# Kernel optimization log

Hardware: AMD Instinct MI355X
Metric: run time of the kernel (lower is better)

Reference implementation:

```python
import jax, jax.numpy as jnp
import numpy as np

BBOX_STD_DEV = jnp.array([0.1, 0.1, 0.2, 0.2], dtype=jnp.float32)
MIN_CONF = 0.15          # hardcoded in source (tf.where(probs >= 0.15))
NMS_THR = 0.3            # config.DETECTION_NMS_THRESHOLD
MAX_INST = 100           # config.DETECTION_MAX_INSTANCES
B, N = 8, 2048


def apply_box_deltas(boxes, deltas):
    # boxes: [N,4] (y1,x1,y2,x2); deltas: [N,4] (dy,dx,log dh,log dw)
    h = boxes[:, 2] - boxes[:, 0]
    w = boxes[:, 3] - boxes[:, 1]
    cy = boxes[:, 0] + 0.5 * h + deltas[:, 0] * h
    cx = boxes[:, 1] + 0.5 * w + deltas[:, 1] * w
    h = h * jnp.exp(deltas[:, 2])
    w = w * jnp.exp(deltas[:, 3])
    y1 = cy - 0.5 * h
    x1 = cx - 0.5 * w
    return jnp.stack([y1, x1, y1 + h, x1 + w], axis=1)


def clip_boxes(boxes, window):
    wy1, wx1, wy2, wx2 = window[0], window[1], window[2], window[3]
    y1 = jnp.clip(boxes[:, 0], wy1, wy2)
    x1 = jnp.clip(boxes[:, 1], wx1, wx2)
    y2 = jnp.clip(boxes[:, 2], wy1, wy2)
    x2 = jnp.clip(boxes[:, 3], wx1, wx2)
    return jnp.stack([y1, x1, y2, x2], axis=1)


def pairwise_iou(boxes):
    # boxes: [N,4] -> iou: [N,N]
    y1, x1, y2, x2 = boxes[:, 0], boxes[:, 1], boxes[:, 2], boxes[:, 3]
    area = (y2 - y1) * (x2 - x1)
    iy1 = jnp.maximum(y1[:, None], y1[None, :])
    ix1 = jnp.maximum(x1[:, None], x1[None, :])
    iy2 = jnp.minimum(y2[:, None], y2[None, :])
    ix2 = jnp.minimum(x2[:, None], x2[None, :])
    inter = jnp.maximum(iy2 - iy1, 0.0) * jnp.maximum(ix2 - ix1, 0.0)
    union = area[:, None] + area[None, :] - inter
    return inter / (union + 1e-8)


def refine_one(rois_i, probs_i, deltas_i, window_i):
    scores = probs_i[:, 0]
    boxes = clip_boxes(apply_box_deltas(rois_i, deltas_i * BBOX_STD_DEV), window_i)
    valid = scores >= MIN_CONF  # confidence filter (mask instead of gather)

    # sort by score descending; greedy NMS over sorted order
    order = jnp.argsort(-scores)
    sb, ss, sv = boxes[order], scores[order], valid[order]
    iou = pairwise_iou(sb)  # [N,N]
    idx = jnp.arange(N)

    def step(kept, xs):
        i, row, v = xs
        suppressed = jnp.any(kept & (idx < i) & (row > NMS_THR))
        return kept.at[i].set(v & ~suppressed), None

    kept, _ = jax.lax.scan(step, jnp.zeros((N,), dtype=bool), (idx, iou, sv))

    # top-k kept by score (already sorted desc, so top_k over masked scores)
    masked = jnp.where(kept, ss, -jnp.inf)
    _, top_i = jax.lax.top_k(masked, MAX_INST)
    ok = kept[top_i]
    det = jnp.concatenate([sb[top_i], ss[top_i][:, None]], axis=1)  # [MAX_INST,5]
    return jnp.where(ok[:, None], det, 0.0)  # zero-pad slots past num kept


def setup_inputs() -> dict:
    key = jax.random.key(0)
    k1, k2, k3 = jax.random.split(key, 3)
    # well-formed normalized rois: y1<y2, x1<x2
    yy = jnp.sort(jax.random.uniform(k1, (B, N, 2)), axis=-1)
    xx = jnp.sort(jax.random.uniform(jax.random.fold_in(k1, 1), (B, N, 2)), axis=-1)
    rois = jnp.stack([yy[..., 0], xx[..., 0], yy[..., 1], xx[..., 1]], axis=-1)
    bbox_scores = jax.random.uniform(k2, (B, N, 1), dtype=jnp.float32)
    deltas = jax.random.normal(k3, (B, N, 4), dtype=jnp.float32) * 0.1
    window = jnp.tile(jnp.array([[0.02, 0.02, 0.98, 0.98]], dtype=jnp.float32), (B, 1))
    return {"rois": rois, "bbox_scores": bbox_scores, "deltas": deltas, "window": window}


def reference(rois, bbox_scores, deltas, window):
    # -> [B, MAX_INST, 5] (y1,x1,y2,x2,score), normalized coords, zero padded
    return jax.vmap(refine_one)(rois, bbox_scores, deltas, window)
```

## Files before the change

### kernel.cpp

```cpp
#include <hip/hip_runtime.h>
#include <math.h>

#define NBOX 2048
#define NBATCH 8
#define MAX_INST 100
#define MIN_CONF 0.15f
#define NMS_THR 0.3f
#define BLOCK 512
#define NWAVE 8

typedef unsigned long long ull;

__device__ inline float4 decode_box(float4 r, float4 d,
                                    float wy1, float wx1, float wy2, float wx2) {
    float h  = __fsub_rn(r.z, r.x);
    float w  = __fsub_rn(r.w, r.y);
    float dy = __fmul_rn(d.x, 0.1f);
    float dx = __fmul_rn(d.y, 0.1f);
    float dh = __fmul_rn(d.z, 0.2f);
    float dw = __fmul_rn(d.w, 0.2f);
    float cy = __fadd_rn(__fadd_rn(r.x, __fmul_rn(0.5f, h)), __fmul_rn(dy, h));
    float cx = __fadd_rn(__fadd_rn(r.y, __fmul_rn(0.5f, w)), __fmul_rn(dx, w));
    float h2 = __fmul_rn(h, expf(dh));
    float w2 = __fmul_rn(w, expf(dw));
    float y1 = __fsub_rn(cy, __fmul_rn(0.5f, h2));
    float x1 = __fsub_rn(cx, __fmul_rn(0.5f, w2));
    float y2 = __fadd_rn(y1, h2);
    float x2 = __fadd_rn(x1, w2);
    float4 b;
    b.x = fminf(fmaxf(y1, wy1), wy2);
    b.y = fminf(fmaxf(x1, wx1), wx2);
    b.z = fminf(fmaxf(y2, wy1), wy2);
    b.w = fminf(fmaxf(x2, wx1), wx2);
    return b;
}

__device__ inline float iou_pa(float ax, float ay, float az, float aw2, float areaA,
                               float4 b, float areaB) {
    float iy1 = fmaxf(ax,  b.x);
    float ix1 = fmaxf(ay,  b.y);
    float iy2 = fminf(az,  b.z);
    float ix2 = fminf(aw2, b.w);
    float ih = fmaxf(__fsub_rn(iy2, iy1), 0.0f);
    float iw = fmaxf(__fsub_rn(ix2, ix1), 0.0f);
    float inter = __fmul_rn(ih, iw);
    float uni = __fadd_rn(__fsub_rn(__fadd_rn(areaA, areaB), inter), 1e-8f);
    return __fdiv_rn(inter, uni);
}

__device__ inline ull shfl_xor64(ull x, int d) {
    unsigned lo = (unsigned)x, hi = (unsigned)(x >> 32);
    lo = __shfl_xor(lo, d);
    hi = __shfl_xor(hi, d);
    return ((ull)hi << 32) | lo;
}

__device__ inline void cmpsel(ull& a, ull& b, bool takeMinA) {
    ull mn = a < b ? a : b;
    ull mx = a < b ? b : a;
    a = takeMinA ? mn : mx;
    b = takeMinA ? mx : mn;
}

__device__ inline float readlane_f(float x, int sl) {
    return __uint_as_float((unsigned)__builtin_amdgcn_readlane((int)__float_as_uint(x), sl));
}

__global__ __launch_bounds__(BLOCK)
void detect_refine_kernel(const float* __restrict__ rois,
                          const float* __restrict__ scores_in,
                          const float* __restrict__ deltas,
                          const float* __restrict__ window,
                          float* __restrict__ out) {
    const int b    = blockIdx.x;
    const int tid  = threadIdx.x;
    const int lane = tid & 63;
    const int wid  = tid >> 6;

    __shared__ ull    keys[NBOX];
    __shared__ float4 sbox[NBOX];
    __shared__ float  sarea[NBOX];
    __shared__ float  sscore[NBOX];
    __shared__ ull    dead8[NWAVE];
    __shared__ float4 skept[MAX_INST];
    __shared__ float  skeptar[MAX_INST];
    __shared__ float  skeptsc[MAX_INST];
    __shared__ int    s_m;

    const float wy1 = window[b * 4 + 0];
    const float wx1 = window[b * 4 + 1];
    const float wy2 = window[b * 4 + 2];
    const float wx2 = window[b * 4 + 3];

    float* outb = out + (size_t)b * MAX_INST * 5;

    const int e0 = tid * 4;
    ull v[4];
    {
        float4 sc = ((const float4*)(scores_in + (size_t)b * NBOX))[tid];
        float s4[4] = {sc.x, sc.y, sc.z, sc.w};
#pragma unroll
        for (int s = 0; s < 4; ++s) {
            unsigned u = __float_as_uint(s4[s]);
            u = (u & 0x80000000u) ? ~u : (u | 0x80000000u);
            v[s] = ((ull)(~u) << 32) | (unsigned)(e0 + s);
        }
    }
    for (unsigned k = 2; k <= NBOX; k <<= 1) {
        if (k >= 512) {
#pragma unroll
            for (int s = 0; s < 4; ++s) keys[e0 + s] = v[s];
            __syncthreads();
            for (unsigned j = k >> 1; j >= 256; j >>= 1) {
                for (int t = tid; t < NBOX / 2; t += BLOCK) {
                    int i = 2 * t - (t & (j - 1));
                    int p = i | j;
                    bool up = ((i & k) == 0);
                    ull a = keys[i], c = keys[p];
                    bool sw = up ? (a > c) : (a < c);
                    if (sw) { keys[i] = c; keys[p] = a; }
                }
                __syncthreads();
            }
#pragma unroll
            for (int s = 0; s < 4; ++s) v[s] = keys[e0 + s];
        }
        unsigned jstart = ((k >> 1) > 128u) ? 128u : (k >> 1);
        for (unsigned j = jstart; j >= 4; j >>= 1) {
            int d = (int)(j >> 2);
#pragma unroll
            for (int s = 0; s < 4; ++s) {
                ull p = shfl_xor64(v[s], d);
                int e = e0 + s;
                bool takeMin = (((e & j) == 0) == ((e & k) == 0));
                v[s] = takeMin ? (v[s] < p ? v[s] : p) : (v[s] > p ? v[s] : p);
            }
        }
        if (k >= 4) {
            bool up = ((e0 & k) == 0);
            cmpsel(v[0], v[2], up);
            cmpsel(v[1], v[3], up);
        }
        {
            bool upA = ((e0 & k) == 0);
            bool upB = (((e0 + 2) & k) == 0);
            cmpsel(v[0], v[1], upA);
            cmpsel(v[2], v[3], upB);
        }
    }

#pragma unroll
    for (int s = 0; s < 4; ++s) {
        int r = e0 + s;
        int oi = (int)(v[s] & 0xFFFFFFFFull);
        float4 rr = ((const float4*)rois)[b * NBOX + oi];
        float4 dd = ((const float4*)deltas)[b * NBOX + oi];
        float4 bb = decode_box(rr, dd, wy1, wx1, wy2, wx2);
        sbox[r]   = bb;
        sarea[r]  = __fmul_rn(__fsub_rn(bb.z, bb.x), __fsub_rn(bb.w, bb.y));
        sscore[r] = scores_in[b * NBOX + oi];
    }
    __syncthreads();

    int count = 0;
    for (int base = 0; base < NBOX && count < MAX_INST; base += 64) {
        float4 cb = sbox[base + lane];
        float  ca = sarea[base + lane];
        float  cs = sscore[base + lane];

        bool deadp = (cs < MIN_CONF);
        {
            int k = wid;
            for (; k + 8 < count; k += 16) {
                float4 k1 = skept[k];     float a1 = skeptar[k];
                float4 k2 = skept[k + 8]; float a2 = skeptar[k + 8];
                deadp |= (iou_pa(k1.x, k1.y, k1.z, k1.w, a1, cb, ca) > NMS_THR);
                deadp |= (iou_pa(k2.x, k2.y, k2.z, k2.w, a2, cb, ca) > NMS_THR);
            }
            if (k < count) {
                float4 k1 = skept[k]; float a1 = skeptar[k];
                deadp |= (iou_pa(k1.x, k1.y, k1.z, k1.w, a1, cb, ca) > NMS_THR);
            }
        }
        ull bal = __ballot(deadp);
        if (lane == 0) dead8[wid] = bal;
        __syncthreads();

        if (wid == 0) {
            ull dead = dead8[0];
#pragma unroll
            for (int q = 1; q < NWAVE; ++q) dead |= dead8[q];
            ull alive = ~dead;
            int m = 0;
            const int maxm = MAX_INST - count;
            while (alive && m < maxm) {
                int il = __builtin_amdgcn_readfirstlane((int)__builtin_ctzll(alive));
                float kx = readlane_f(cb.x, il);
                float ky = readlane_f(cb.y, il);
                float kz = readlane_f(cb.z, il);
                float kw = readlane_f(cb.w, il);
                float ka = readlane_f(ca,   il);
                float ks = readlane_f(cs,   il);
                if (lane == 0) {
                    skept[count + m]   = make_float4(kx, ky, kz, kw);
                    skeptar[count + m] = ka;
                    skeptsc[count + m] = ks;
                }
                ++m;
                ull sup = __ballot(iou_pa(kx, ky, kz, kw, ka, cb, ca) > NMS_THR);
                alive &= ~sup;
                alive &= ~(1ull << il);
            }
            if (lane == 0) s_m = m;
        }
        __syncthreads();
        count += s_m;
    }

    for (int i = tid; i < MAX_INST * 5; i += BLOCK) {
        int r = i / 5, c = i % 5;
        float vv = 0.0f;
        if (r < count) {
            float4 kb = skept[r];
            vv = (c == 0) ? kb.x
               : (c == 1) ? kb.y
               : (c == 2) ? kb.z
               : (c == 3) ? kb.w
               :            skeptsc[r];
        }
        outb[i] = vv;
    }
}

extern "C" void kernel_launch(void* const* d_in, const int* in_sizes, int n_in,
                              void* d_out, int out_size, void* d_ws, size_t ws_size,
                              hipStream_t stream) {
    const float* rois    = (const float*)d_in[0];
    const float* scores  = (const float*)d_in[1];
    const float* deltas  = (const float*)d_in[2];
    const float* window  = (const float*)d_in[3];
    float* out = (float*)d_out;
    detect_refine_kernel<<<NBATCH, BLOCK, 0, stream>>>(rois, scores, deltas, window, out);
}
```

Baseline: 49.44 us.

## Pipeline NMS windows: waves 1-7 pre-check next window while wave 0 resolves current

Restructures the windowed greedy NMS so that wave 0 resolves window w while waves 1-7 concurrently compute suppression of window w+1 against boxes kept up to window w-1. Wave 0 then checks only the boxes kept in the previous window, held in registers and broadcast with readlane. This halves the number of block barriers per window and overlaps the serial scan with the parallel pre-check. Kept-box areas are recomputed instead of stored, and the loop runs over double-buffered shared state, which adds complexity and extra per-window readlane work in wave 0.

```diff
diff --git a/kernel.cpp b/kernel.cpp
--- a/kernel.cpp
+++ b/kernel.cpp
@@ -7,7 +7,7 @@
 #define MIN_CONF 0.15f
 #define NMS_THR 0.3f
 #define BLOCK 512
-#define NWAVE 8
+#define NWIN 32
 
 typedef unsigned long long ull;
 
@@ -48,6 +48,10 @@
     return __fdiv_rn(inter, uni);
 }
 
+__device__ inline float area_of(float4 a) {
+    return __fmul_rn(__fsub_rn(a.z, a.x), __fsub_rn(a.w, a.y));
+}
+
 __device__ inline ull shfl_xor64(ull x, int d) {
     unsigned lo = (unsigned)x, hi = (unsigned)(x >> 32);
     lo = __shfl_xor(lo, d);
@@ -81,11 +85,12 @@
     __shared__ float4 sbox[NBOX];
     __shared__ float  sarea[NBOX];
     __shared__ float  sscore[NBOX];
-    __shared__ ull    dead8[NWAVE];
+    __shared__ ull    sdead[2][7];
     __shared__ float4 skept[MAX_INST];
-    __shared__ float  skeptar[MAX_INST];
     __shared__ float  skeptsc[MAX_INST];
-    __shared__ int    s_m;
+    __shared__ int    s_cnt[2];
+    __shared__ int    s_stop[2];
+    __shared__ int    s_final;
 
     const float wy1 = window[b * 4 + 0];
     const float wx1 = window[b * 4 + 1];
@@ -157,39 +162,41 @@
         float4 dd = ((const float4*)deltas)[b * NBOX + oi];
         float4 bb = decode_box(rr, dd, wy1, wx1, wy2, wx2);
         sbox[r]   = bb;
-        sarea[r]  = __fmul_rn(__fsub_rn(bb.z, bb.x), __fsub_rn(bb.w, bb.y));
+        sarea[r]  = area_of(bb);
         sscore[r] = scores_in[b * NBOX + oi];
     }
+    if (tid == 0) { s_cnt[0] = 0; s_stop[0] = 0; s_stop[1] = 0; s_final = 0; }
     __syncthreads();
 
     int count = 0;
-    for (int base = 0; base < NBOX && count < MAX_INST; base += 64) {
-        float4 cb = sbox[base + lane];
-        float  ca = sarea[base + lane];
-        float  cs = sscore[base + lane];
-
-        bool deadp = (cs < MIN_CONF);
-        {
-            int k = wid;
-            for (; k + 8 < count; k += 16) {
-                float4 k1 = skept[k];     float a1 = skeptar[k];
-                float4 k2 = skept[k + 8]; float a2 = skeptar[k + 8];
-                deadp |= (iou_pa(k1.x, k1.y, k1.z, k1.w, a1, cb, ca) > NMS_THR);
-                deadp |= (iou_pa(k2.x, k2.y, k2.z, k2.w, a2, cb, ca) > NMS_THR);
-            }
-            if (k < count) {
-                float4 k1 = skept[k]; float a1 = skeptar[k];
-                deadp |= (iou_pa(k1.x, k1.y, k1.z, k1.w, a1, cb, ca) > NMS_THR);
-            }
-        }
-        ull bal = __ballot(deadp);
-        if (lane == 0) dead8[wid] = bal;
-        __syncthreads();
+    float4 pk;  float pka = 0.f;
+    int m_prev = 0;
+
+    for (int w = 0; w < NWIN; ++w) {
+        const int par = w & 1, pnx = par ^ 1;
 
         if (wid == 0) {
-            ull dead = dead8[0];
-#pragma unroll
-            for (int q = 1; q < NWAVE; ++q) dead |= dead8[q];
+            float4 cb = sbox[(w << 6) + lane];
+            float  ca = sarea[(w << 6) + lane];
+            float  cs = sscore[(w << 6) + lane];
+
+            ull dead;
+            if (w == 0) {
+                dead = __ballot(cs < MIN_CONF);
+            } else {
+                dead = sdead[par][0];
+#pragma unroll
+                for (int q = 1; q < 7; ++q) dead |= sdead[par][q];
+            }
+            for (int j = 0; j < m_prev; ++j) {
+                float kx = readlane_f(pk.x, j);
+                float ky = readlane_f(pk.y, j);
+                float kz = readlane_f(pk.z, j);
+                float kw = readlane_f(pk.w, j);
+                float ka = readlane_f(pka,  j);
+                dead |= __ballot(iou_pa(kx, ky, kz, kw, ka, cb, ca) > NMS_THR);
+            }
+
             ull alive = ~dead;
             int m = 0;
             const int maxm = MAX_INST - count;
@@ -203,24 +210,55 @@
                 float ks = readlane_f(cs,   il);
                 if (lane == 0) {
                     skept[count + m]   = make_float4(kx, ky, kz, kw);
-                    skeptar[count + m] = ka;
                     skeptsc[count + m] = ks;
                 }
+                if (lane == m) { pk = make_float4(kx, ky, kz, kw); pka = ka; }
                 ++m;
                 ull sup = __ballot(iou_pa(kx, ky, kz, kw, ka, cb, ca) > NMS_THR);
                 alive &= ~sup;
                 alive &= ~(1ull << il);
             }
-            if (lane == 0) s_m = m;
+            m_prev = m;
+            count += m;
+            if (lane == 0) {
+                s_cnt[pnx]  = count;
+                s_stop[par] = (count >= MAX_INST) || (w + 1 >= NWIN);
+                s_final     = count;
+            }
+        } else if (w + 1 < NWIN) {
+            const int nw = ((w + 1) << 6) + lane;
+            float4 cb = sbox[nw];
+            float  ca = sarea[nw];
+            float  cs = sscore[nw];
+            const int cnt = s_cnt[par];
+            bool dp = (cs < MIN_CONF);
+            int k = wid - 1;
+            for (; k + 21 < cnt; k += 28) {
+                float4 a0 = skept[k];
+                float4 a1 = skept[k + 7];
+                float4 a2 = skept[k + 14];
+                float4 a3 = skept[k + 21];
+                dp |= (iou_pa(a0.x, a0.y, a0.z, a0.w, area_of(a0), cb, ca) > NMS_THR);
+                dp |= (iou_pa(a1.x, a1.y, a1.z, a1.w, area_of(a1), cb, ca) > NMS_THR);
+                dp |= (iou_pa(a2.x, a2.y, a2.z, a2.w, area_of(a2), cb, ca) > NMS_THR);
+                dp |= (iou_pa(a3.x, a3.y, a3.z, a3.w, area_of(a3), cb, ca) > NMS_THR);
+            }
+            for (; k < cnt; k += 7) {
+                float4 a0 = skept[k];
+                dp |= (iou_pa(a0.x, a0.y, a0.z, a0.w, area_of(a0), cb, ca) > NMS_THR);
+            }
+            ull bal = __ballot(dp);
+            if (lane == 0) sdead[pnx][wid - 1] = bal;
         }
         __syncthreads();
-        count += s_m;
-    }
-
+        if (s_stop[par]) break;
+    }
+
+    const int fin = s_final;
     for (int i = tid; i < MAX_INST * 5; i += BLOCK) {
         int r = i / 5, c = i % 5;
         float vv = 0.0f;
-        if (r < count) {
+        if (r < fin) {
             float4 kb = skept[r];
             vv = (c == 0) ? kb.x
                : (c == 1) ? kb.y
```

After: 59.92 us. +21.2%, slower.
